# Optimization experiments

Hardware: AMD Instinct MI355X
Metric: run time of the kernel (lower is better)

## Reference

```python
import jax, jax.numpy as jnp
import numpy as np

B, LQ, LK = 8, 2048, 2048
DQ = DK = DI = DV = 1024
SCALE = 1.0 / np.sqrt(DK).astype(np.float32)  # (sqrt(1/sqrt(dk)))^2 applied to q and k
NEG_INF = float('-inf')


def setup_inputs() -> dict:
    key = jax.random.key(0)
    ks = jax.random.split(key, 6)
    return {
        'query': jax.random.normal(ks[0], (B, LQ, DQ), dtype=jnp.float32),
        'key': jax.random.normal(ks[1], (B, LK, DK), dtype=jnp.float32),
        'value': jax.random.normal(ks[2], (B, LK, DV), dtype=jnp.float32),
        'mask': jax.random.randint(ks[3], (B, 1, LK), 0, 2, dtype=jnp.int32),
        'Wq': jax.random.normal(ks[4], (DI, DQ), dtype=jnp.float32) / np.sqrt(DQ),
        'Wk': jax.random.normal(ks[5], (DI, DK), dtype=jnp.float32) / np.sqrt(DK),
    }


def reference(query, key, value, mask, Wq, Wk):
    # Linear projections (bias=False): y = x @ W^T
    q = jnp.einsum('bld,ed->ble', query, Wq)           # [B,LQ,DI]
    k = jnp.einsum('bld,ed->ble', key, Wk)             # [B,LK,DI]
    scores = jnp.einsum('bqe,bke->bqk', q, k) * SCALE  # [B,LQ,LK]
    scores = scores.astype(jnp.float32)
    scores = jnp.where(mask == 0, NEG_INF, scores)     # mask broadcasts [B,1,LK]
    attn_weight = jax.nn.softmax(scores, axis=-1)      # fp32 softmax, dropout p=0 -> identity
    attn_cxt = jnp.einsum('bqk,bkd->bqd', attn_weight, value)
    return attn_cxt, attn_weight
```

## Files before the change

### kernel.cpp

```cpp
#include <hip/hip_runtime.h>


typedef __bf16 bf16x8 __attribute__((ext_vector_type(8)));
typedef float  f32x4  __attribute__((ext_vector_type(4)));

#define AS1 __attribute__((address_space(1)))
#define AS3 __attribute__((address_space(3)))

__device__ __forceinline__ ushort f2bf(float f) {
  union { float f; unsigned u; } v; v.f = f;
  unsigned u = v.u;
  unsigned r = (u + 0x7FFFu + ((u >> 16) & 1u)) >> 16;
  return (ushort)r;
}

constexpr float SCORE_SCALE = 0.03125f;

template <int MODE>
__global__ __launch_bounds__(512, 2)
void gemm_bt(const ushort* __restrict__ Ag, const ushort* __restrict__ Bg,
             void* __restrict__ Cv, const int* __restrict__ mask,
             int N, int K, long sA, long sB, long sC, int sMask)
{
  __shared__ ushort As[2][256 * 64];
  __shared__ ushort Bs[2][256 * 64];

  const int nx = gridDim.x, ny = gridDim.y, nz = gridDim.z;
  const long nwg = (long)nx * ny * nz;
  long flat = blockIdx.x + (long)nx * (blockIdx.y + (long)ny * blockIdx.z);
  int bx = blockIdx.x, by = blockIdx.y, bz = blockIdx.z;
  if ((nwg & 7) == 0) {
    const long cpx = nwg >> 3;
    flat = (flat & 7) * cpx + (flat >> 3);
    bx = (int)(flat % nx);
    by = (int)((flat / nx) % ny);
    bz = (int)(flat / ((long)nx * ny));
  }
  const int m0 = by * 256;
  const int n0 = bx * 256;

  const ushort* Ab = Ag + (long)bz * sA;
  const ushort* Bb = Bg + (long)bz * sB;

  const int tid  = threadIdx.x;
  const int lane = tid & 63;
  const int wid  = tid >> 6;
  const int wm   = wid >> 2;
  const int wn   = wid & 3;
  const int l15  = lane & 15;
  const int lq   = lane >> 4;

  long gAoff[4], gBoff[4];
  int  ldsoff[4];
#pragma unroll
  for (int j = 0; j < 4; ++j) {
    const int idx = j * 512 + tid;
    const int row = idx >> 3;
    const int lc  = (idx & 7) ^ (row & 7);
    gAoff[j]  = (long)(m0 + row) * K + lc * 8;
    gBoff[j]  = (long)(n0 + row) * K + lc * 8;
    ldsoff[j] = (j * 512 + wid * 64) * 8;
  }

  f32x4 acc[8][4];
#pragma unroll
  for (int i = 0; i < 8; ++i)
#pragma unroll
    for (int j = 0; j < 4; ++j) acc[i][j] = (f32x4){0.f, 0.f, 0.f, 0.f};

  const int nt = K >> 6;

#pragma unroll
  for (int j = 0; j < 4; ++j)
    __builtin_amdgcn_global_load_lds((const AS1 void*)(Ab + gAoff[j]),
                                     (AS3 void*)(&As[0][ldsoff[j]]), 16, 0, 0);
#pragma unroll
  for (int j = 0; j < 4; ++j)
    __builtin_amdgcn_global_load_lds((const AS1 void*)(Bb + gBoff[j]),
                                     (AS3 void*)(&Bs[0][ldsoff[j]]), 16, 0, 0);

  const int arow0 = wm * 128 + l15;
  const int brow0 = wn * 64 + l15;

  for (int t = 0; t < nt; ++t) {
    const ushort* Abuf = As[t & 1];
    const ushort* Bbuf = Bs[t & 1];

    if (t + 1 < nt) {
      const long ko = (long)(t + 1) * 64;
      const int  nb = (t + 1) & 1;
#pragma unroll
      for (int j = 0; j < 4; ++j)
        __builtin_amdgcn_global_load_lds((const AS1 void*)(Ab + gAoff[j] + ko),
                                         (AS3 void*)(&As[nb][ldsoff[j]]), 16, 0, 0);
#pragma unroll
      for (int j = 0; j < 4; ++j)
        __builtin_amdgcn_global_load_lds((const AS1 void*)(Bb + gBoff[j] + ko),
                                         (AS3 void*)(&Bs[nb][ldsoff[j]]), 16, 0, 0);
      asm volatile("s_waitcnt vmcnt(8)" ::: "memory");
    } else {
      asm volatile("s_waitcnt vmcnt(0)" ::: "memory");
    }
    __builtin_amdgcn_sched_barrier(0);
    __builtin_amdgcn_s_barrier();
    __builtin_amdgcn_sched_barrier(0);

#pragma unroll
    for (int kk = 0; kk < 2; ++kk) {
      bf16x8 bfr[4];
#pragma unroll
      for (int ni = 0; ni < 4; ++ni) {
        const int row = brow0 + ni * 16;
        const int pc  = (kk * 4 + lq) ^ (row & 7);
        bfr[ni] = *(const bf16x8*)(Bbuf + row * 64 + pc * 8);
      }
      __builtin_amdgcn_s_setprio(1);
#pragma unroll
      for (int mi = 0; mi < 8; ++mi) {
        const int row = arow0 + mi * 16;
        const int pc  = (kk * 4 + lq) ^ (row & 7);
        const bf16x8 a = *(const bf16x8*)(Abuf + row * 64 + pc * 8);
#pragma unroll
        for (int ni = 0; ni < 4; ++ni)
          acc[mi][ni] = __builtin_amdgcn_mfma_f32_16x16x32_bf16(
              a, bfr[ni], acc[mi][ni], 0, 0, 0);
      }
      __builtin_amdgcn_s_setprio(0);
    }
    __builtin_amdgcn_sched_barrier(0);
    __builtin_amdgcn_s_barrier();
  }

  const int rbase = lq * 4;
  if constexpr (MODE == 0) {
    ushort* C = (ushort*)Cv + (long)bz * sC;
#pragma unroll
    for (int mi = 0; mi < 8; ++mi) {
      const int r0 = m0 + wm * 128 + mi * 16 + rbase;
#pragma unroll
      for (int ni = 0; ni < 4; ++ni) {
        const int col = n0 + wn * 64 + ni * 16 + l15;
#pragma unroll
        for (int r = 0; r < 4; ++r)
          C[(long)(r0 + r) * N + col] = f2bf(acc[mi][ni][r]);
      }
    }
  } else if constexpr (MODE == 1) {
    float* C = (float*)Cv + (long)bz * sC;
    const int* mb = mask + (long)bz * sMask;
    int coln[4], mk[4];
#pragma unroll
    for (int ni = 0; ni < 4; ++ni) {
      coln[ni] = n0 + wn * 64 + ni * 16 + l15;
      mk[ni]   = mb[coln[ni]];
    }
    const float ninf = -__builtin_inff();
#pragma unroll
    for (int mi = 0; mi < 8; ++mi) {
      const int r0 = m0 + wm * 128 + mi * 16 + rbase;
#pragma unroll
      for (int ni = 0; ni < 4; ++ni)
#pragma unroll
        for (int r = 0; r < 4; ++r)
          C[(long)(r0 + r) * N + coln[ni]] =
              mk[ni] ? acc[mi][ni][r] * SCORE_SCALE : ninf;
    }
  } else {
    float* C = (float*)Cv + (long)bz * sC;
#pragma unroll
    for (int mi = 0; mi < 8; ++mi) {
      const int r0 = m0 + wm * 128 + mi * 16 + rbase;
#pragma unroll
      for (int ni = 0; ni < 4; ++ni) {
        const int col = n0 + wn * 64 + ni * 16 + l15;
#pragma unroll
        for (int r = 0; r < 4; ++r)
          C[(long)(r0 + r) * N + col] = acc[mi][ni][r];
      }
    }
  }
}

__global__ __launch_bounds__(256)
void cvt_f32_bf16(const float* __restrict__ in, ushort* __restrict__ out, int n4)
{
  const int i = blockIdx.x * 256 + threadIdx.x;
  if (i >= n4) return;
  float4 v = ((const float4*)in)[i];
  ushort4 o;
  o.x = f2bf(v.x); o.y = f2bf(v.y); o.z = f2bf(v.z); o.w = f2bf(v.w);
  ((ushort4*)out)[i] = o;
}

__global__ __launch_bounds__(256)
void transpose_v(const float* __restrict__ V, ushort* __restrict__ Vt)
{
  __shared__ ushort t[64][65];
  const int b = blockIdx.z;
  const float* Vb  = V  + (long)b * 2048 * 1024;
  ushort*      Vtb = Vt + (long)b * 1024 * 2048;
  const int k0 = blockIdx.x * 64, d0 = blockIdx.y * 64;
  const int c  = threadIdx.x & 63;
  const int r4 = threadIdx.x >> 6;
#pragma unroll
  for (int i = 0; i < 64; i += 4)
    t[i + r4][c] = f2bf(Vb[(long)(k0 + i + r4) * 1024 + d0 + c]);
  __syncthreads();
#pragma unroll
  for (int i = 0; i < 64; i += 4)
    Vtb[(long)(d0 + i + r4) * 2048 + k0 + c] = t[c][i + r4];
}

__global__ __launch_bounds__(256)
void softmax_rows(float* __restrict__ S, ushort* __restrict__ Wb)
{
  const long row = blockIdx.x;
  float*  Sr = S  + row * 2048;
  ushort* Wr = Wb + row * 2048;
  const int tid = threadIdx.x;

  float4 a = *(const float4*)(Sr + tid * 4);
  float4 c = *(const float4*)(Sr + 1024 + tid * 4);

  float m = fmaxf(fmaxf(fmaxf(a.x, a.y), fmaxf(a.z, a.w)),
                  fmaxf(fmaxf(c.x, c.y), fmaxf(c.z, c.w)));
#pragma unroll
  for (int off = 32; off > 0; off >>= 1) m = fmaxf(m, __shfl_xor(m, off, 64));

  __shared__ float red[8];
  const int wid = tid >> 6, lane = tid & 63;
  if (lane == 0) red[wid] = m;
  __syncthreads();
  m = fmaxf(fmaxf(red[0], red[1]), fmaxf(red[2], red[3]));

  float e[8];
  e[0] = __expf(a.x - m); e[1] = __expf(a.y - m);
  e[2] = __expf(a.z - m); e[3] = __expf(a.w - m);
  e[4] = __expf(c.x - m); e[5] = __expf(c.y - m);
  e[6] = __expf(c.z - m); e[7] = __expf(c.w - m);
  float s = e[0] + e[1] + e[2] + e[3] + e[4] + e[5] + e[6] + e[7];
#pragma unroll
  for (int off = 32; off > 0; off >>= 1) s += __shfl_xor(s, off, 64);
  if (lane == 0) red[4 + wid] = s;
  __syncthreads();
  s = red[4] + red[5] + red[6] + red[7];

  const float inv = 1.0f / s;
  float4 o0 = make_float4(e[0] * inv, e[1] * inv, e[2] * inv, e[3] * inv);
  float4 o1 = make_float4(e[4] * inv, e[5] * inv, e[6] * inv, e[7] * inv);
  *(float4*)(Sr + tid * 4)        = o0;
  *(float4*)(Sr + 1024 + tid * 4) = o1;
  ushort4 w0, w1;
  w0.x = f2bf(o0.x); w0.y = f2bf(o0.y); w0.z = f2bf(o0.z); w0.w = f2bf(o0.w);
  w1.x = f2bf(o1.x); w1.y = f2bf(o1.y); w1.z = f2bf(o1.z); w1.w = f2bf(o1.w);
  *(ushort4*)(Wr + tid * 4)        = w0;
  *(ushort4*)(Wr + 1024 + tid * 4) = w1;
}

constexpr size_t SZ_XB  = 16384UL * 1024 * 2;
constexpr size_t OFF_QB = 0;
constexpr size_t OFF_KB = SZ_XB;
constexpr size_t OFF_WQ = 2 * SZ_XB;
constexpr size_t OFF_WK = OFF_WQ + 1024UL * 1024 * 2;
constexpr size_t OFF_QP = OFF_WK + 1024UL * 1024 * 2;
constexpr size_t OFF_KP = OFF_QP + SZ_XB;
constexpr size_t OFF_VT = OFF_KP + SZ_XB;
constexpr size_t OFF_WB = 0;

extern "C" void kernel_launch(void* const* d_in, const int* in_sizes, int n_in,
                              void* d_out, int out_size, void* d_ws, size_t ws_size,
                              hipStream_t stream)
{
  (void)in_sizes; (void)n_in; (void)out_size; (void)ws_size;

  const float* query = (const float*)d_in[0];
  const float* key   = (const float*)d_in[1];
  const float* value = (const float*)d_in[2];
  const int*   mask  = (const int*)d_in[3];
  const float* Wq    = (const float*)d_in[4];
  const float* Wk    = (const float*)d_in[5];

  float* out_cxt = (float*)d_out;
  float* out_w   = out_cxt + 8L * 2048 * 1024;

  char* ws = (char*)d_ws;
  ushort* qb  = (ushort*)(ws + OFF_QB);
  ushort* kb  = (ushort*)(ws + OFF_KB);
  ushort* wqb = (ushort*)(ws + OFF_WQ);
  ushort* wkb = (ushort*)(ws + OFF_WK);
  ushort* Qp  = (ushort*)(ws + OFF_QP);
  ushort* Kp  = (ushort*)(ws + OFF_KP);
  ushort* Vt  = (ushort*)(ws + OFF_VT);
  ushort* Wb  = (ushort*)(ws + OFF_WB);

  cvt_f32_bf16<<<16384, 256, 0, stream>>>(query, qb, 4194304);
  cvt_f32_bf16<<<16384, 256, 0, stream>>>(key,   kb, 4194304);
  cvt_f32_bf16<<<1024,  256, 0, stream>>>(Wq, wqb, 262144);
  cvt_f32_bf16<<<1024,  256, 0, stream>>>(Wk, wkb, 262144);
  transpose_v<<<dim3(32, 16, 8), 256, 0, stream>>>(value, Vt);

  gemm_bt<0><<<dim3(4, 64, 1), 512, 0, stream>>>(qb, wqb, Qp, nullptr,
                                                 1024, 1024, 0, 0, 0, 0);
  gemm_bt<0><<<dim3(4, 64, 1), 512, 0, stream>>>(kb, wkb, Kp, nullptr,
                                                 1024, 1024, 0, 0, 0, 0);

  gemm_bt<1><<<dim3(8, 8, 8), 512, 0, stream>>>(Qp, Kp, out_w, mask,
                                                2048, 1024,
                                                2048L * 1024, 2048L * 1024,
                                                2048L * 2048, 2048);

  softmax_rows<<<16384, 256, 0, stream>>>(out_w, Wb);

  gemm_bt<2><<<dim3(4, 8, 8), 512, 0, stream>>>(Wb, Vt, out_cxt, nullptr,
                                                1024, 2048,
                                                2048L * 2048, 1024L * 2048,
                                                2048L * 1024, 0);
}
```

Before: 640.4 us.

## Split GEMM tiles into half-quadrants with fine-grained staged load/MFMA interleaving

Restructures the shared-memory tiles of the bf16 GEMM into two 128-row halves per operand. The main loop is unrolled by two K-steps and issued as four quadrant MFMA phases, with global-to-LDS staging of the next halves placed between them, bracketed by barriers in a ping-pong style. The wave-to-output mapping also changes so that each wave covers interleaved 16-row and 16-column strips across the quadrants. The aim is to overlap memory loads with MFMA work at finer granularity and cut LDS stalls, at the cost of many more barriers and a more complex vmcnt accounting.

```diff
diff --git a/kernel.cpp b/kernel.cpp
--- a/kernel.cpp
+++ b/kernel.cpp
@@ -22,8 +22,8 @@
              void* __restrict__ Cv, const int* __restrict__ mask,
              int N, int K, long sA, long sB, long sC, int sMask)
 {
-  __shared__ ushort As[2][256 * 64];
-  __shared__ ushort Bs[2][256 * 64];
+  __shared__ ushort As[2][2][8192];
+  __shared__ ushort Bs[2][2][8192];
 
   const int nx = gridDim.x, ny = gridDim.y, nz = gridDim.z;
   const long nwg = (long)nx * ny * nz;
@@ -50,99 +50,128 @@
   const int l15  = lane & 15;
   const int lq   = lane >> 4;
 
-  long gAoff[4], gBoff[4];
-  int  ldsoff[4];
-#pragma unroll
-  for (int j = 0; j < 4; ++j) {
-    const int idx = j * 512 + tid;
-    const int row = idx >> 3;
-    const int lc  = (idx & 7) ^ (row & 7);
-    gAoff[j]  = (long)(m0 + row) * K + lc * 8;
-    gBoff[j]  = (long)(n0 + row) * K + lc * 8;
-    ldsoff[j] = (j * 512 + wid * 64) * 8;
+  const int srow = tid >> 3;
+  const int sxor = ((tid & 7) ^ (srow & 7)) * 8;
+  long gAoff[2][2], gBoff[2][2];
+#pragma unroll
+  for (int h = 0; h < 2; ++h)
+#pragma unroll
+    for (int j = 0; j < 2; ++j) {
+      gAoff[h][j] = (long)(m0 + h * 128 + j * 64 + srow) * K + sxor;
+      gBoff[h][j] = (long)(n0 + h * 128 + j * 64 + srow) * K + sxor;
+    }
+  const int ldso0 = wid * 512;
+  const int ldso1 = 4096 + wid * 512;
+
+  int arowb[4], browb[2], pc8[2];
+#pragma unroll
+  for (int i = 0; i < 4; ++i) arowb[i] = (i * 32 + wm * 16 + l15) * 64;
+#pragma unroll
+  for (int i = 0; i < 2; ++i) browb[i] = (i * 64 + wn * 16 + l15) * 64;
+#pragma unroll
+  for (int kk = 0; kk < 2; ++kk) pc8[kk] = ((kk * 4 + lq) ^ (lane & 7)) * 8;
+
+  f32x4 acc[8][4];
+#pragma unroll
+  for (int i = 0; i < 8; ++i)
+#pragma unroll
+    for (int j = 0; j < 4; ++j) acc[i][j] = (f32x4){0.f, 0.f, 0.f, 0.f};
+
+  bf16x8 af[4][2], bA[2][2], bB[2][2];
+
+#define STAGE_A(T_, H, NB) do { const long ko_ = (long)(T_) * 64;             \
+    __builtin_amdgcn_global_load_lds((const AS1 void*)(Ab + gAoff[H][0] + ko_),\
+                                     (AS3 void*)(&As[NB][H][ldso0]), 16, 0, 0);\
+    __builtin_amdgcn_global_load_lds((const AS1 void*)(Ab + gAoff[H][1] + ko_),\
+                                     (AS3 void*)(&As[NB][H][ldso1]), 16, 0, 0);\
+  } while (0)
+#define STAGE_B(T_, H, NB) do { const long ko_ = (long)(T_) * 64;             \
+    __builtin_amdgcn_global_load_lds((const AS1 void*)(Bb + gBoff[H][0] + ko_),\
+                                     (AS3 void*)(&Bs[NB][H][ldso0]), 16, 0, 0);\
+    __builtin_amdgcn_global_load_lds((const AS1 void*)(Bb + gBoff[H][1] + ko_),\
+                                     (AS3 void*)(&Bs[NB][H][ldso1]), 16, 0, 0);\
+  } while (0)
+#define LD_A(MH, NB) do {                                                     \
+    _Pragma("unroll") for (int mi2 = 0; mi2 < 4; ++mi2)                        \
+    _Pragma("unroll") for (int kk = 0; kk < 2; ++kk)                           \
+      af[mi2][kk] = *(const bf16x8*)(&As[NB][MH][arowb[mi2] + pc8[kk]]);       \
+  } while (0)
+#define LD_B(DST, NH, NB) do {                                                \
+    _Pragma("unroll") for (int ni2 = 0; ni2 < 2; ++ni2)                        \
+    _Pragma("unroll") for (int kk = 0; kk < 2; ++kk)                           \
+      DST[ni2][kk] = *(const bf16x8*)(&Bs[NB][NH][browb[ni2] + pc8[kk]]);      \
+  } while (0)
+#define QMFMA(MH, NH, BB) do {                                                \
+    __builtin_amdgcn_s_setprio(1);                                             \
+    _Pragma("unroll") for (int kk = 0; kk < 2; ++kk)                           \
+    _Pragma("unroll") for (int mi2 = 0; mi2 < 4; ++mi2)                        \
+    _Pragma("unroll") for (int ni2 = 0; ni2 < 2; ++ni2)                        \
+      acc[(MH)*4 + mi2][(NH)*2 + ni2] =                                        \
+          __builtin_amdgcn_mfma_f32_16x16x32_bf16(                             \
+              af[mi2][kk], BB[ni2][kk], acc[(MH)*4 + mi2][(NH)*2 + ni2],       \
+              0, 0, 0);                                                        \
+    __builtin_amdgcn_s_setprio(0);                                             \
+  } while (0)
+#define BARX do { __builtin_amdgcn_sched_barrier(0);                          \
+    __builtin_amdgcn_s_barrier(); __builtin_amdgcn_sched_barrier(0); } while (0)
+
+  const int nt    = K >> 6;
+  const int niter = nt >> 1;
+
+  STAGE_A(0, 0, 0); STAGE_B(0, 0, 0); STAGE_B(0, 1, 0); STAGE_A(0, 1, 0);
+  STAGE_A(1, 0, 1); STAGE_B(1, 1, 1);
+  asm volatile("s_waitcnt vmcnt(4)" ::: "memory");
+  BARX;
+
+  for (int it = 0; it < niter; ++it) {
+    const int  T  = it * 2;
+    const bool pf = (it + 1 < niter);
+    LD_A(0, 0); LD_B(bA, 0, 0);
+    STAGE_A(T + 1, 1, 1);
+    BARX; QMFMA(0, 0, bA); BARX;
+    LD_B(bB, 1, 0);
+    STAGE_B(T + 1, 0, 1);
+    BARX; QMFMA(0, 1, bB); BARX;
+    LD_A(1, 0);
+    if (pf) STAGE_A(T + 2, 0, 0);
+    BARX; QMFMA(1, 1, bB); BARX;
+    if (pf) { STAGE_B(T + 2, 1, 0);
+              asm volatile("s_waitcnt vmcnt(4)" ::: "memory"); }
+    else    { asm volatile("s_waitcnt vmcnt(0)" ::: "memory"); }
+    BARX; QMFMA(1, 0, bA); BARX;
+    LD_A(0, 1); LD_B(bA, 0, 1);
+    if (pf) STAGE_A(T + 2, 1, 0);
+    BARX; QMFMA(0, 0, bA); BARX;
+    LD_B(bB, 1, 1);
+    if (pf) STAGE_B(T + 2, 0, 0);
+    BARX; QMFMA(0, 1, bB); BARX;
+    LD_A(1, 1);
+    if (pf) STAGE_A(T + 3, 0, 1);
+    BARX; QMFMA(1, 1, bB); BARX;
+    if (pf) { STAGE_B(T + 3, 1, 1);
+              asm volatile("s_waitcnt vmcnt(4)" ::: "memory"); }
+    BARX; QMFMA(1, 0, bA); BARX;
   }
 
-  f32x4 acc[8][4];
-#pragma unroll
-  for (int i = 0; i < 8; ++i)
-#pragma unroll
-    for (int j = 0; j < 4; ++j) acc[i][j] = (f32x4){0.f, 0.f, 0.f, 0.f};
-
-  const int nt = K >> 6;
-
-#pragma unroll
-  for (int j = 0; j < 4; ++j)
-    __builtin_amdgcn_global_load_lds((const AS1 void*)(Ab + gAoff[j]),
-                                     (AS3 void*)(&As[0][ldsoff[j]]), 16, 0, 0);
-#pragma unroll
-  for (int j = 0; j < 4; ++j)
-    __builtin_amdgcn_global_load_lds((const AS1 void*)(Bb + gBoff[j]),
-                                     (AS3 void*)(&Bs[0][ldsoff[j]]), 16, 0, 0);
-
-  const int arow0 = wm * 128 + l15;
-  const int brow0 = wn * 64 + l15;
-
-  for (int t = 0; t < nt; ++t) {
-    const ushort* Abuf = As[t & 1];
-    const ushort* Bbuf = Bs[t & 1];
-
-    if (t + 1 < nt) {
-      const long ko = (long)(t + 1) * 64;
-      const int  nb = (t + 1) & 1;
-#pragma unroll
-      for (int j = 0; j < 4; ++j)
-        __builtin_amdgcn_global_load_lds((const AS1 void*)(Ab + gAoff[j] + ko),
-                                         (AS3 void*)(&As[nb][ldsoff[j]]), 16, 0, 0);
-#pragma unroll
-      for (int j = 0; j < 4; ++j)
-        __builtin_amdgcn_global_load_lds((const AS1 void*)(Bb + gBoff[j] + ko),
-                                         (AS3 void*)(&Bs[nb][ldsoff[j]]), 16, 0, 0);
-      asm volatile("s_waitcnt vmcnt(8)" ::: "memory");
-    } else {
-      asm volatile("s_waitcnt vmcnt(0)" ::: "memory");
-    }
-    __builtin_amdgcn_sched_barrier(0);
-    __builtin_amdgcn_s_barrier();
-    __builtin_amdgcn_sched_barrier(0);
-
-#pragma unroll
-    for (int kk = 0; kk < 2; ++kk) {
-      bf16x8 bfr[4];
-#pragma unroll
-      for (int ni = 0; ni < 4; ++ni) {
-        const int row = brow0 + ni * 16;
-        const int pc  = (kk * 4 + lq) ^ (row & 7);
-        bfr[ni] = *(const bf16x8*)(Bbuf + row * 64 + pc * 8);
-      }
-      __builtin_amdgcn_s_setprio(1);
-#pragma unroll
-      for (int mi = 0; mi < 8; ++mi) {
-        const int row = arow0 + mi * 16;
-        const int pc  = (kk * 4 + lq) ^ (row & 7);
-        const bf16x8 a = *(const bf16x8*)(Abuf + row * 64 + pc * 8);
-#pragma unroll
-        for (int ni = 0; ni < 4; ++ni)
-          acc[mi][ni] = __builtin_amdgcn_mfma_f32_16x16x32_bf16(
-              a, bfr[ni], acc[mi][ni], 0, 0, 0);
-      }
-      __builtin_amdgcn_s_setprio(0);
-    }
-    __builtin_amdgcn_sched_barrier(0);
-    __builtin_amdgcn_s_barrier();
-  }
+#undef STAGE_A
+#undef STAGE_B
+#undef LD_A
+#undef LD_B
+#undef QMFMA
+#undef BARX
 
   const int rbase = lq * 4;
   if constexpr (MODE == 0) {
     ushort* C = (ushort*)Cv + (long)bz * sC;
 #pragma unroll
-    for (int mi = 0; mi < 8; ++mi) {
-      const int r0 = m0 + wm * 128 + mi * 16 + rbase;
-#pragma unroll
-      for (int ni = 0; ni < 4; ++ni) {
-        const int col = n0 + wn * 64 + ni * 16 + l15;
+    for (int i = 0; i < 8; ++i) {
+      const int r0 = m0 + (i >> 2) * 128 + (i & 3) * 32 + wm * 16 + rbase;
+#pragma unroll
+      for (int j = 0; j < 4; ++j) {
+        const int col = n0 + (j >> 1) * 128 + (j & 1) * 64 + wn * 16 + l15;
 #pragma unroll
         for (int r = 0; r < 4; ++r)
-          C[(long)(r0 + r) * N + col] = f2bf(acc[mi][ni][r]);
+          C[(long)(r0 + r) * N + col] = f2bf(acc[i][j][r]);
       }
     }
   } else if constexpr (MODE == 1) {
@@ -150,32 +179,32 @@
     const int* mb = mask + (long)bz * sMask;
     int coln[4], mk[4];
 #pragma unroll
-    for (int ni = 0; ni < 4; ++ni) {
-      coln[ni] = n0 + wn * 64 + ni * 16 + l15;
-      mk[ni]   = mb[coln[ni]];
+    for (int j = 0; j < 4; ++j) {
+      coln[j] = n0 + (j >> 1) * 128 + (j & 1) * 64 + wn * 16 + l15;
+      mk[j]   = mb[coln[j]];
     }
     const float ninf = -__builtin_inff();
 #pragma unroll
-    for (int mi = 0; mi < 8; ++mi) {
-      const int r0 = m0 + wm * 128 + mi * 16 + rbase;
-#pragma unroll
-      for (int ni = 0; ni < 4; ++ni)
+    for (int i = 0; i < 8; ++i) {
+      const int r0 = m0 + (i >> 2) * 128 + (i & 3) * 32 + wm * 16 + rbase;
+#pragma unroll
+      for (int j = 0; j < 4; ++j)
 #pragma unroll
         for (int r = 0; r < 4; ++r)
-          C[(long)(r0 + r) * N + coln[ni]] =
-              mk[ni] ? acc[mi][ni][r] * SCORE_SCALE : ninf;
+          C[(long)(r0 + r) * N + coln[j]] =
+              mk[j] ? acc[i][j][r] * SCORE_SCALE : ninf;
     }
   } else {
     float* C = (float*)Cv + (long)bz * sC;
 #pragma unroll
-    for (int mi = 0; mi < 8; ++mi) {
-      const int r0 = m0 + wm * 128 + mi * 16 + rbase;
-#pragma unroll
-      for (int ni = 0; ni < 4; ++ni) {
-        const int col = n0 + wn * 64 + ni * 16 + l15;
+    for (int i = 0; i < 8; ++i) {
+      const int r0 = m0 + (i >> 2) * 128 + (i & 3) * 32 + wm * 16 + rbase;
+#pragma unroll
+      for (int j = 0; j < 4; ++j) {
+        const int col = n0 + (j >> 1) * 128 + (j & 1) * 64 + wn * 16 + l15;
 #pragma unroll
         for (int r = 0; r < 4; ++r)
-          C[(long)(r0 + r) * N + col] = acc[mi][ni][r];
+          C[(long)(r0 + r) * N + col] = acc[i][j][r];
       }
     }
   }
```

Result: faster. 614.0 us (-4.1%).
